# Kernel optimization log

Hardware: AMD Instinct MI355X
Metric: run time of the kernel (lower is better)

Reference implementation:

```python
import jax, jax.numpy as jnp
import numpy as np

E, D, A = 1024, 1024, 512

def setup_inputs() -> dict:
    key = jax.random.key(0)
    ks = jax.random.split(key, 8)
    B, S = 32, 2048
    s_e = 1.0 / np.sqrt(E)
    s_d = 1.0 / np.sqrt(D)
    s_a = 1.0 / np.sqrt(A)
    return {
        "encoder_outputs": jax.random.normal(ks[0], (B, S, E), jnp.float32),
        "decoder_hidden": jax.random.normal(ks[1], (B, D), jnp.float32),
        "We": jax.random.uniform(ks[2], (E, A), jnp.float32, -s_e, s_e),
        "be": jax.random.uniform(ks[3], (A,), jnp.float32, -s_e, s_e),
        "Wd": jax.random.uniform(ks[4], (D, A), jnp.float32, -s_d, s_d),
        "bd": jax.random.uniform(ks[5], (A,), jnp.float32, -s_d, s_d),
        "v_w": jax.random.uniform(ks[6], (A,), jnp.float32, -s_a, s_a),
        "v_b": jax.random.uniform(ks[7], (), jnp.float32, -s_a, s_a),
    }

def reference(encoder_outputs, decoder_hidden, We, be, Wd, bd, v_w, v_b):
    # encoder_energy: [B,S,A]; decoder_energy: [B,1,A]
    enc_e = jnp.einsum('bse,ea->bsa', encoder_outputs, We) + be
    dec_e = (decoder_hidden @ Wd + bd)[:, None, :]
    energy = jnp.tanh(enc_e + dec_e)                     # [B,S,A]
    scores = jnp.einsum('bsa,a->bs', energy, v_w) + v_b  # [B,S]
    attn = jax.nn.softmax(scores, axis=1)                # [B,S]
    context = jnp.einsum('bs,bse->be', attn, encoder_outputs)  # [B,E]
    return context, attn
```

## Files before the change

### kernel.cpp

```cpp
#include <hip/hip_runtime.h>
#include <math.h>

#define E_DIM 1024
#define D_DIM 1024
#define A_DIM 512
#define B_NUM 32
#define S_DIM 2048
#define M_DIM (B_NUM * S_DIM)

typedef unsigned short ushort;
typedef short short8 __attribute__((ext_vector_type(8)));
typedef float f32x4 __attribute__((ext_vector_type(4)));
typedef unsigned short ushort4v __attribute__((ext_vector_type(4)));

typedef const void __attribute__((address_space(1))) cglobal_t;
typedef void __attribute__((address_space(3))) lds_t;

__device__ __forceinline__ void gload_lds16(const void* g, void* l) {
    __builtin_amdgcn_global_load_lds((cglobal_t*)g, (lds_t*)l, 16, 0, 0);
}

__device__ __forceinline__ ushort f2bf(float x) {
    unsigned u = __float_as_uint(x);
    u += 0x7FFF + ((u >> 16) & 1);
    return (ushort)(u >> 16);
}

__device__ __forceinline__ unsigned cvt_pk_bf16(float lo, float hi) {
    unsigned r;
    asm("v_cvt_pk_bf16_f32 %0, %1, %2" : "=v"(r) : "v"(lo), "v"(hi));
    return r;
}

__device__ __forceinline__ float fast_tanh(float x) {
    const float e = __expf(2.0f * x);
    return 1.0f - 2.0f * __builtin_amdgcn_rcpf(e + 1.0f);
}

__global__ __launch_bounds__(256) void k0_dec_energy(
    const float* __restrict__ dh, const float* __restrict__ Wd,
    const float* __restrict__ bd, const float* __restrict__ be,
    float* __restrict__ dec2) {
    __shared__ float sdh[D_DIM];
    const int b = blockIdx.y;
    const int t = threadIdx.x;
    for (int i = t; i < D_DIM; i += 256) sdh[i] = dh[b * D_DIM + i];
    __syncthreads();
    const int a = blockIdx.x * 256 + t;
    float acc = bd[a] + be[a];
#pragma unroll 8
    for (int e = 0; e < D_DIM; ++e) acc += sdh[e] * Wd[(size_t)e * A_DIM + a];
    dec2[b * A_DIM + a] = acc;
}

__global__ __launch_bounds__(256) void k0b_cvt_we(
    const float* __restrict__ We, ushort* __restrict__ Wt) {
    const int n = blockIdx.x;
    const int k0 = threadIdx.x * 4;
    ushort4v v;
#pragma unroll
    for (int j = 0; j < 4; ++j) v[j] = f2bf(We[(size_t)(k0 + j) * A_DIM + n]);
    *reinterpret_cast<ushort4v*>(&Wt[(size_t)n * E_DIM + k0]) = v;
}

#define BM4 128
#define BN4 256
#define NT4 32
#define BUFU4 12288

__global__ __launch_bounds__(256, 2) void k1_fused(
    const float* __restrict__ enc, const ushort* __restrict__ Wt,
    const float* __restrict__ dec2, const float* __restrict__ v_w,
    float* __restrict__ pscores) {
    __shared__ ushort L[2 * BUFU4];

    const int t = threadIdx.x;
    const int l = t & 63;
    const int w = t >> 6;
    const int wm = w >> 1, wn = w & 1;
    const int fr = l & 15;
    const int kg = l >> 4;

    const int o = ((blockIdx.x & 7) << 7) | (blockIdx.x >> 3);
    const int x = o >> 1, ny = o & 1;
    const int row0 = x * BM4;
    const int n0 = ny * BN4;
    const int b = row0 >> 11;

    const int arow = t >> 1;
    const int ac0 = (t & 1) * 2;
    const float* Asrc = enc + (size_t)(row0 + arow) * E_DIM + ac0 * 8;
    const int aswz0 = arow * 64 + ((ac0 ^ ((arow >> 1) & 3)) << 4);
    const int aswz1 = arow * 64 + (((ac0 + 1) ^ ((arow >> 1) & 3)) << 4);

    const ushort* BsrcQ[4];
#pragma unroll
    for (int q = 0; q < 4; ++q) {
        const int row = q * 64 + w * 16 + (l >> 2);
        const int c = (l & 3) ^ ((row >> 1) & 3);
        BsrcQ[q] = Wt + (size_t)(n0 + row) * E_DIM + c * 8;
    }

    f32x4 acc[4][8];
#pragma unroll
    for (int i = 0; i < 4; ++i)
#pragma unroll
        for (int j = 0; j < 8; ++j) acc[i][j] = (f32x4){0.f, 0.f, 0.f, 0.f};

    float4 pa[4];

#define LOADA4(ktv)                                                            \
    {                                                                          \
        pa[0] = *reinterpret_cast<const float4*>(Asrc + (ktv) * 32);           \
        pa[1] = *reinterpret_cast<const float4*>(Asrc + (ktv) * 32 + 4);       \
        pa[2] = *reinterpret_cast<const float4*>(Asrc + (ktv) * 32 + 8);       \
        pa[3] = *reinterpret_cast<const float4*>(Asrc + (ktv) * 32 + 12);      \
    }

#define STAGEB4(cb, ktv)                                                       \
    {                                                                          \
        _Pragma("unroll") for (int q = 0; q < 4; ++q)                          \
            gload_lds16(BsrcQ[q] + (ktv) * 32,                                 \
                        L + (cb) * BUFU4 + 4096 + (q * 64 + w * 16) * 32);     \
    }

#define WRITEA4(cb)                                                            \
    {                                                                          \
        const unsigned u0 = cvt_pk_bf16(pa[0].x, pa[0].y);                     \
        const unsigned u1 = cvt_pk_bf16(pa[0].z, pa[0].w);                     \
        const unsigned u2 = cvt_pk_bf16(pa[1].x, pa[1].y);                     \
        const unsigned u3 = cvt_pk_bf16(pa[1].z, pa[1].w);                     \
        const unsigned u4 = cvt_pk_bf16(pa[2].x, pa[2].y);                     \
        const unsigned u5 = cvt_pk_bf16(pa[2].z, pa[2].w);                     \
        const unsigned u6 = cvt_pk_bf16(pa[3].x, pa[3].y);                     \
        const unsigned u7 = cvt_pk_bf16(pa[3].z, pa[3].w);                     \
        *reinterpret_cast<int4*>((char*)L + (cb) * 24576 + aswz0) =            \
            make_int4(u0, u1, u2, u3);                                         \
        *reinterpret_cast<int4*>((char*)L + (cb) * 24576 + aswz1) =            \
            make_int4(u4, u5, u6, u7);                                         \
    }

    LOADA4(0);
    STAGEB4(0, 0);
    asm volatile("s_waitcnt vmcnt(4)" ::: "memory");
    WRITEA4(0);
    __syncthreads();

    for (int kt = 0; kt < NT4; ++kt) {
        const int cur = kt & 1;
        if (kt < NT4 - 1) {
            LOADA4(kt + 1);
            STAGEB4(cur ^ 1, kt + 1);
        }

        const char* Ab = (const char*)L + cur * 24576;
        const char* Bb = Ab + 8192;
        short8 af[4], bf[8];
#pragma unroll
        for (int i = 0; i < 4; ++i) {
            const int r = wm * 64 + i * 16 + fr;
            af[i] = *reinterpret_cast<const short8*>(
                Ab + r * 64 + ((kg ^ ((r >> 1) & 3)) << 4));
        }
#pragma unroll
        for (int j = 0; j < 8; ++j) {
            const int r = wn * 128 + j * 16 + fr;
            bf[j] = *reinterpret_cast<const short8*>(
                Bb + r * 64 + ((kg ^ ((r >> 1) & 3)) << 4));
        }
        __builtin_amdgcn_s_setprio(1);
#pragma unroll
        for (int i = 0; i < 4; ++i)
#pragma unroll
            for (int j = 0; j < 8; ++j)
                acc[i][j] = __builtin_amdgcn_mfma_f32_16x16x32_bf16(af[i], bf[j], acc[i][j], 0, 0, 0);
        __builtin_amdgcn_s_setprio(0);

        if (kt < NT4 - 1) {
            asm volatile("s_waitcnt vmcnt(4)" ::: "memory");
            WRITEA4(cur ^ 1);
        }
        __syncthreads();
    }

    float rowsum[4][4];
#pragma unroll
    for (int i = 0; i < 4; ++i)
#pragma unroll
        for (int r = 0; r < 4; ++r) rowsum[i][r] = 0.0f;

#pragma unroll
    for (int j = 0; j < 8; ++j) {
        const int ag = n0 + wn * 128 + j * 16 + fr;
        const float bias = dec2[b * A_DIM + ag];
        const float vw = v_w[ag];
#pragma unroll
        for (int i = 0; i < 4; ++i)
#pragma unroll
            for (int r = 0; r < 4; ++r)
                rowsum[i][r] += fast_tanh(acc[i][j][r] + bias) * vw;
    }
#pragma unroll
    for (int m = 1; m < 16; m <<= 1)
#pragma unroll
        for (int i = 0; i < 4; ++i)
#pragma unroll
            for (int r = 0; r < 4; ++r)
                rowsum[i][r] += __shfl_xor(rowsum[i][r], m, 64);

    __syncthreads();
    float* red = reinterpret_cast<float*>(L);
    if (fr == 0) {
#pragma unroll
        for (int i = 0; i < 4; ++i)
#pragma unroll
            for (int r = 0; r < 4; ++r)
                red[(wm * 64 + i * 16 + kg * 4 + r) * 2 + wn] = rowsum[i][r];
    }
    __syncthreads();
    if (t < BM4)
        pscores[(size_t)(row0 + t) * 2 + ny] = red[t * 2] + red[t * 2 + 1];
}

__global__ __launch_bounds__(256) void k2_softmax(
    const float* __restrict__ pscores, const float* __restrict__ v_b,
    float* __restrict__ attn_out, int W) {
    __shared__ float sc[S_DIM];
    __shared__ float red[8];
    const int b = blockIdx.x;
    const int t = threadIdx.x;
    const int wave = t >> 6, lane = t & 63;
    const float vb = v_b[0];

    float lmax = -1e30f;
    for (int s = t; s < S_DIM; s += 256) {
        float v = vb;
        for (int c = 0; c < W; ++c) v += pscores[(size_t)(b * S_DIM + s) * W + c];
        sc[s] = v;
        lmax = fmaxf(lmax, v);
    }
#pragma unroll
    for (int off = 32; off > 0; off >>= 1) lmax = fmaxf(lmax, __shfl_down(lmax, off, 64));
    if (lane == 0) red[wave] = lmax;
    __syncthreads();
    const float bmax = fmaxf(fmaxf(red[0], red[1]), fmaxf(red[2], red[3]));

    float lsum = 0.0f;
    for (int s = t; s < S_DIM; s += 256) {
        const float e = expf(sc[s] - bmax);
        sc[s] = e;
        lsum += e;
    }
#pragma unroll
    for (int off = 32; off > 0; off >>= 1) lsum += __shfl_down(lsum, off, 64);
    if (lane == 0) red[4 + wave] = lsum;
    __syncthreads();
    const float inv = 1.0f / (red[4] + red[5] + red[6] + red[7]);
    for (int s = t; s < S_DIM; s += 256) attn_out[b * S_DIM + s] = sc[s] * inv;
}

#define SC_CHUNK 128
#define N_SC (S_DIM / SC_CHUNK)
__global__ __launch_bounds__(256) void k3_ctx_partial(
    const float* __restrict__ enc, const float* __restrict__ attn,
    float* __restrict__ pctx) {
    const int b = blockIdx.y;
    const int scb = blockIdx.x;
    const int t = threadIdx.x;
    const int s0 = scb * SC_CHUNK;
    float4 acc = {0.0f, 0.0f, 0.0f, 0.0f};
    const float4* encv =
        reinterpret_cast<const float4*>(enc + (size_t)(b * S_DIM + s0) * E_DIM);
#pragma unroll 4
    for (int s = 0; s < SC_CHUNK; ++s) {
        const float w = attn[b * S_DIM + s0 + s];
        const float4 v = encv[(size_t)s * (E_DIM / 4) + t];
        acc.x += w * v.x;
        acc.y += w * v.y;
        acc.z += w * v.z;
        acc.w += w * v.w;
    }
    *reinterpret_cast<float4*>(&pctx[(size_t)(b * N_SC + scb) * E_DIM + t * 4]) = acc;
}

__global__ __launch_bounds__(256) void k4_ctx_reduce(
    const float* __restrict__ pctx, float* __restrict__ ctx) {
    const int b = blockIdx.x;
    const int t = threadIdx.x;
    float4 acc = {0.0f, 0.0f, 0.0f, 0.0f};
#pragma unroll
    for (int s = 0; s < N_SC; ++s) {
        const float4 v = *reinterpret_cast<const float4*>(
            &pctx[(size_t)(b * N_SC + s) * E_DIM + t * 4]);
        acc.x += v.x;
        acc.y += v.y;
        acc.z += v.z;
        acc.w += v.w;
    }
    *reinterpret_cast<float4*>(&ctx[(size_t)b * E_DIM + t * 4]) = acc;
}

extern "C" void kernel_launch(void* const* d_in, const int* in_sizes, int n_in,
                              void* d_out, int out_size, void* d_ws, size_t ws_size,
                              hipStream_t stream) {
    (void)in_sizes; (void)n_in; (void)out_size; (void)ws_size;
    const float* enc = (const float*)d_in[0];
    const float* dh  = (const float*)d_in[1];
    const float* We  = (const float*)d_in[2];
    const float* be  = (const float*)d_in[3];
    const float* Wd  = (const float*)d_in[4];
    const float* bd  = (const float*)d_in[5];
    const float* vw  = (const float*)d_in[6];
    const float* vb  = (const float*)d_in[7];

    float* out = (float*)d_out;
    float* ctx_out = out;
    float* attn_out = out + B_NUM * E_DIM;

    float* ws = (float*)d_ws;
    float* dec2    = ws;
    float* pscores = ws + 16384;
    float* pctx    = ws + 16384 + 131072;
    ushort* Wt     = (ushort*)(ws + 16384 + 131072 + 524288);

    k0_dec_energy<<<dim3(2, 32), 256, 0, stream>>>(dh, Wd, bd, be, dec2);
    k0b_cvt_we<<<dim3(A_DIM), 256, 0, stream>>>(We, Wt);
    k1_fused<<<dim3((M_DIM / BM4) * (A_DIM / BN4)), 256, 0, stream>>>(
        enc, Wt, dec2, vw, pscores);
    k2_softmax<<<dim3(B_NUM), 256, 0, stream>>>(pscores, vb, attn_out, 2);
    k3_ctx_partial<<<dim3(N_SC, B_NUM), 256, 0, stream>>>(enc, attn_out, pctx);
    k4_ctx_reduce<<<dim3(B_NUM), 256, 0, stream>>>(pctx, ctx_out);
}
```

Baseline: 221.0 us.

## Shrink fused GEMM N-tile to 128 and raise occupancy to three blocks

The fused encoder-energy GEMM now uses 128x128 tiles instead of 128x256. Accumulators per thread and LDS per block are halved, which allows launch bounds of three blocks per CU. The A-tile load is remapped so each thread reads four rows with 8-byte LDS stores, and partial scores are split four ways across N, so softmax reduces four partials. The cost is that the fp32 encoder rows are now read and converted twice as often, since the grid has four N tiles instead of two.

Result: slower. 228.0 us (+3.2%).

```diff
diff --git a/kernel.cpp b/kernel.cpp
--- a/kernel.cpp
+++ b/kernel.cpp
@@ -12,6 +12,7 @@
 typedef short short8 __attribute__((ext_vector_type(8)));
 typedef float f32x4 __attribute__((ext_vector_type(4)));
 typedef unsigned short ushort4v __attribute__((ext_vector_type(4)));
+typedef unsigned int uint2v __attribute__((ext_vector_type(2)));
 
 typedef const void __attribute__((address_space(1))) cglobal_t;
 typedef void __attribute__((address_space(3))) lds_t;
@@ -63,16 +64,15 @@
     *reinterpret_cast<ushort4v*>(&Wt[(size_t)n * E_DIM + k0]) = v;
 }
 
-#define BM4 128
-#define BN4 256
-#define NT4 32
-#define BUFU4 12288
-
-__global__ __launch_bounds__(256, 2) void k1_fused(
+#define BM5 128
+#define BN5 128
+#define NT5 32
+
+__global__ __launch_bounds__(256, 3) void k1_fused(
     const float* __restrict__ enc, const ushort* __restrict__ Wt,
     const float* __restrict__ dec2, const float* __restrict__ v_w,
     float* __restrict__ pscores) {
-    __shared__ ushort L[2 * BUFU4];
+    __shared__ ushort L[2 * 8192];
 
     const int t = threadIdx.x;
     const int l = t & 63;
@@ -81,81 +81,78 @@
     const int fr = l & 15;
     const int kg = l >> 4;
 
-    const int o = ((blockIdx.x & 7) << 7) | (blockIdx.x >> 3);
-    const int x = o >> 1, ny = o & 1;
-    const int row0 = x * BM4;
-    const int n0 = ny * BN4;
+    const int o = ((blockIdx.x & 7) << 8) | (blockIdx.x >> 3);
+    const int x = o >> 2, y = o & 3;
+    const int row0 = x * BM5;
+    const int n0 = y * BN5;
     const int b = row0 >> 11;
 
-    const int arow = t >> 1;
-    const int ac0 = (t & 1) * 2;
-    const float* Asrc = enc + (size_t)(row0 + arow) * E_DIM + ac0 * 8;
-    const int aswz0 = arow * 64 + ((ac0 ^ ((arow >> 1) & 3)) << 4);
-    const int aswz1 = arow * 64 + (((ac0 + 1) ^ ((arow >> 1) & 3)) << 4);
-
-    const ushort* BsrcQ[4];
-#pragma unroll
-    for (int q = 0; q < 4; ++q) {
+    const int arow = t >> 3;
+    const int achk = t & 7;
+    const float* AsrcT = enc + (size_t)(row0 + arow) * E_DIM + achk * 4;
+    const int aswzc = ((((achk >> 1) ^ ((t >> 4) & 3)) << 4) | ((t & 1) << 3));
+    const int awbase = arow * 64 + aswzc;
+
+    const ushort* BsrcQ[2];
+#pragma unroll
+    for (int q = 0; q < 2; ++q) {
         const int row = q * 64 + w * 16 + (l >> 2);
         const int c = (l & 3) ^ ((row >> 1) & 3);
         BsrcQ[q] = Wt + (size_t)(n0 + row) * E_DIM + c * 8;
     }
 
-    f32x4 acc[4][8];
+    f32x4 acc[4][4];
 #pragma unroll
     for (int i = 0; i < 4; ++i)
 #pragma unroll
-        for (int j = 0; j < 8; ++j) acc[i][j] = (f32x4){0.f, 0.f, 0.f, 0.f};
+        for (int j = 0; j < 4; ++j) acc[i][j] = (f32x4){0.f, 0.f, 0.f, 0.f};
 
     float4 pa[4];
 
-#define LOADA4(ktv)                                                            \
-    {                                                                          \
-        pa[0] = *reinterpret_cast<const float4*>(Asrc + (ktv) * 32);           \
-        pa[1] = *reinterpret_cast<const float4*>(Asrc + (ktv) * 32 + 4);       \
-        pa[2] = *reinterpret_cast<const float4*>(Asrc + (ktv) * 32 + 8);       \
-        pa[3] = *reinterpret_cast<const float4*>(Asrc + (ktv) * 32 + 12);      \
-    }
-
-#define STAGEB4(cb, ktv)                                                       \
+#define LOADA5(ktv)                                                            \
     {                                                                          \
         _Pragma("unroll") for (int q = 0; q < 4; ++q)                          \
+            pa[q] = *reinterpret_cast<const float4*>(                          \
+                AsrcT + (size_t)q * 32 * E_DIM + (ktv) * 32);                  \
+    }
+
+#define STAGEB5(cb, ktv)                                                       \
+    {                                                                          \
+        _Pragma("unroll") for (int q = 0; q < 2; ++q)                          \
             gload_lds16(BsrcQ[q] + (ktv) * 32,                                 \
-                        L + (cb) * BUFU4 + 4096 + (q * 64 + w * 16) * 32);     \
-    }
-
-#define WRITEA4(cb)                                                            \
+                        L + (cb) * 8192 + 4096 + (q * 64 + w * 16) * 32);      \
+    }
+
+#define WRITEA5(cb)                                                            \
     {                                                                          \
-        const unsigned u0 = cvt_pk_bf16(pa[0].x, pa[0].y);                     \
-        const unsigned u1 = cvt_pk_bf16(pa[0].z, pa[0].w);                     \
-        const unsigned u2 = cvt_pk_bf16(pa[1].x, pa[1].y);                     \
-        const unsigned u3 = cvt_pk_bf16(pa[1].z, pa[1].w);                     \
-        const unsigned u4 = cvt_pk_bf16(pa[2].x, pa[2].y);                     \
-        const unsigned u5 = cvt_pk_bf16(pa[2].z, pa[2].w);                     \
-        const unsigned u6 = cvt_pk_bf16(pa[3].x, pa[3].y);                     \
-        const unsigned u7 = cvt_pk_bf16(pa[3].z, pa[3].w);                     \
-        *reinterpret_cast<int4*>((char*)L + (cb) * 24576 + aswz0) =            \
-            make_int4(u0, u1, u2, u3);                                         \
-        *reinterpret_cast<int4*>((char*)L + (cb) * 24576 + aswz1) =            \
-            make_int4(u4, u5, u6, u7);                                         \
-    }
-
-    LOADA4(0);
-    STAGEB4(0, 0);
-    asm volatile("s_waitcnt vmcnt(4)" ::: "memory");
-    WRITEA4(0);
-    __syncthreads();
-
-    for (int kt = 0; kt < NT4; ++kt) {
+        _Pragma("unroll") for (int q = 0; q < 4; ++q) {                        \
+            uint2v v2;                                                         \
+            v2[0] = cvt_pk_bf16(pa[q].x, pa[q].y);                             \
+            v2[1] = cvt_pk_bf16(pa[q].z, pa[q].w);                             \
+            *reinterpret_cast<uint2v*>(                                        \
+                (char*)L + (cb) * 16384 + q * 2048 + awbase) = v2;             \
+        }                                                                      \
+    }
+
+#define WAITV(n) asm volatile("s_waitcnt vmcnt(" #n ")" ::: "memory")
+
+    LOADA5(0);
+    STAGEB5(0, 0);
+    WAITV(2);
+    WRITEA5(0);
+    __syncthreads();
+
+    for (int kt = 0; kt < NT5; ++kt) {
         const int cur = kt & 1;
-        if (kt < NT4 - 1) {
-            LOADA4(kt + 1);
-            STAGEB4(cur ^ 1, kt + 1);
+
+        if (kt < NT5 - 1) {
+            LOADA5(kt + 1);
+            STAGEB5(cur ^ 1, kt + 1);
         }
 
-        const char* Ab = (const char*)L + cur * 24576;
+        const char* Ab = (const char*)L + cur * 16384;
         const char* Bb = Ab + 8192;
-        short8 af[4], bf[8];
+        short8 af[4], bf[4];
 #pragma unroll
         for (int i = 0; i < 4; ++i) {
             const int r = wm * 64 + i * 16 + fr;
@@ -163,8 +160,8 @@
                 Ab + r * 64 + ((kg ^ ((r >> 1) & 3)) << 4));
         }
 #pragma unroll
-        for (int j = 0; j < 8; ++j) {
-            const int r = wn * 128 + j * 16 + fr;
+        for (int j = 0; j < 4; ++j) {
+            const int r = wn * 64 + j * 16 + fr;
             bf[j] = *reinterpret_cast<const short8*>(
                 Bb + r * 64 + ((kg ^ ((r >> 1) & 3)) << 4));
         }
@@ -172,13 +169,13 @@
 #pragma unroll
         for (int i = 0; i < 4; ++i)
 #pragma unroll
-            for (int j = 0; j < 8; ++j)
+            for (int j = 0; j < 4; ++j)
                 acc[i][j] = __builtin_amdgcn_mfma_f32_16x16x32_bf16(af[i], bf[j], acc[i][j], 0, 0, 0);
         __builtin_amdgcn_s_setprio(0);
 
-        if (kt < NT4 - 1) {
-            asm volatile("s_waitcnt vmcnt(4)" ::: "memory");
-            WRITEA4(cur ^ 1);
+        if (kt < NT5 - 1) {
+            WAITV(2);
+            WRITEA5(cur ^ 1);
         }
         __syncthreads();
     }
@@ -190,8 +187,8 @@
         for (int r = 0; r < 4; ++r) rowsum[i][r] = 0.0f;
 
 #pragma unroll
-    for (int j = 0; j < 8; ++j) {
-        const int ag = n0 + wn * 128 + j * 16 + fr;
+    for (int j = 0; j < 4; ++j) {
+        const int ag = n0 + wn * 64 + j * 16 + fr;
         const float bias = dec2[b * A_DIM + ag];
         const float vw = v_w[ag];
 #pragma unroll
@@ -218,8 +215,8 @@
                 red[(wm * 64 + i * 16 + kg * 4 + r) * 2 + wn] = rowsum[i][r];
     }
     __syncthreads();
-    if (t < BM4)
-        pscores[(size_t)(row0 + t) * 2 + ny] = red[t * 2] + red[t * 2 + 1];
+    if (t < BM5)
+        pscores[(size_t)(row0 + t) * 4 + y] = red[t * 2] + red[t * 2 + 1];
 }
 
 __global__ __launch_bounds__(256) void k2_softmax(
@@ -320,14 +317,14 @@
     float* ws = (float*)d_ws;
     float* dec2    = ws;
     float* pscores = ws + 16384;
-    float* pctx    = ws + 16384 + 131072;
-    ushort* Wt     = (ushort*)(ws + 16384 + 131072 + 524288);
+    float* pctx    = ws + 16384 + 262144;
+    ushort* Wt     = (ushort*)(ws + 16384 + 262144 + 524288);
 
     k0_dec_energy<<<dim3(2, 32), 256, 0, stream>>>(dh, Wd, bd, be, dec2);
     k0b_cvt_we<<<dim3(A_DIM), 256, 0, stream>>>(We, Wt);
-    k1_fused<<<dim3((M_DIM / BM4) * (A_DIM / BN4)), 256, 0, stream>>>(
+    k1_fused<<<dim3((M_DIM / BM5) * (A_DIM / BN5)), 256, 0, stream>>>(
         enc, Wt, dec2, vw, pscores);
-    k2_softmax<<<dim3(B_NUM), 256, 0, stream>>>(pscores, vb, attn_out, 2);
+    k2_softmax<<<dim3(B_NUM), 256, 0, stream>>>(pscores, vb, attn_out, 4);
     k3_ctx_partial<<<dim3(N_SC, B_NUM), 256, 0, stream>>>(enc, attn_out, pctx);
     k4_ctx_reduce<<<dim3(B_NUM), 256, 0, stream>>>(pctx, ctx_out);
 }
```
